# Kernel optimization log

Measured on AMD Instinct MI355X. Metric: run time of the kernel, lower is better.

The kernel has to match this reference:

```python
import jax, jax.numpy as jnp
import numpy as np

B, NN, HIS, MSG = 16, 1000, 12, 64
NODE_DIM, EDGE_DIM, META_DIM = 32, 16, 128
GAT_DIM = HIS * MSG            # 768
META_IN = NODE_DIM + GAT_DIM   # 800
N = B * NN                     # 16000 total nodes
E = 128000
NEG_SLOPE = 0.2


def setup_inputs() -> dict:
    key = jax.random.key(0)
    ks = jax.random.split(key, 16)
    def glorot(k, shape):
        fan_in = shape[0]
        lim = 1.0 / np.sqrt(fan_in)
        return jax.random.uniform(k, shape, jnp.float32, -lim, lim)
    return {
        "node_feature": jax.random.normal(ks[0], (B, NN, NODE_DIM), jnp.float32),
        "edge_attr": jax.random.normal(ks[1], (E, EDGE_DIM), jnp.float32),
        "message_feature": jax.random.normal(ks[2], (B, NN, HIS, MSG), jnp.float32),
        "edge_index": jax.random.randint(ks[3], (2, E), 0, N, jnp.int64) if jax.config.jax_enable_x64 else jax.random.randint(ks[3], (2, E), 0, N, jnp.int32),
        # node_learner / edge_learner
        "W_node": glorot(ks[4], (NODE_DIM, NODE_DIM)),
        "b_node": jnp.zeros((NODE_DIM,), jnp.float32),
        "W_edge": glorot(ks[5], (EDGE_DIM, EDGE_DIM)),
        "b_edge": jnp.zeros((EDGE_DIM,), jnp.float32),
        # GATConv(768, 768, heads=1, concat=False)
        "W_gat": glorot(ks[6], (GAT_DIM, GAT_DIM)),
        "att_src": glorot(ks[7], (GAT_DIM,)) * 0.1,
        "att_dst": glorot(ks[8], (GAT_DIM,)) * 0.1,
        "b_gat": jnp.zeros((GAT_DIM,), jnp.float32),
        # GNNConv([meta_in, meta_dim], dim=edge_dim)
        "W_nbr": glorot(ks[9], (2 * META_IN + EDGE_DIM, META_DIM)),
        "b_nbr": jnp.zeros((META_DIM,), jnp.float32),
        "W_self": glorot(ks[10], (META_IN, META_DIM)),
        "b_self": jnp.zeros((META_DIM,), jnp.float32),
    }


def reference(node_feature, edge_attr, message_feature, edge_index,
              W_node, b_node, W_edge, b_edge,
              W_gat, att_src, att_dst, b_gat,
              W_nbr, b_nbr, W_self, b_self):
    src, dst = edge_index[0], edge_index[1]  # j -> i

    # node / edge learners
    nf = (node_feature @ W_node + b_node).reshape(-1, NODE_DIM)        # [N, 32]
    ea = edge_attr @ W_edge + b_edge                                   # [E, 16]
    mf = message_feature.reshape(-1, GAT_DIM)                          # [N, 768]

    # --- GATConv (1 head, concat=False, add_self_loops=True, eval: no dropout) ---
    loops = jnp.arange(N, dtype=src.dtype)
    src_sl = jnp.concatenate([src, loops])
    dst_sl = jnp.concatenate([dst, loops])
    h = mf @ W_gat                                                     # [N, 768]
    a_src = h @ att_src                                                # [N]
    a_dst = h @ att_dst                                                # [N]
    alpha = jax.nn.leaky_relu(a_src[src_sl] + a_dst[dst_sl], NEG_SLOPE)  # [E+N]
    amax = jax.ops.segment_max(alpha, dst_sl, num_segments=N)
    ex = jnp.exp(alpha - amax[dst_sl])
    denom = jax.ops.segment_sum(ex, dst_sl, num_segments=N)
    coef = ex / denom[dst_sl]
    gat_out = jax.ops.segment_sum(h[src_sl] * coef[:, None], dst_sl, num_segments=N) + b_gat

    # --- meta input + GNNConv (aggr='add', batch_norm=False) ---
    x = jnp.concatenate([gat_out, nf], axis=-1)                        # [N, 800]
    z = jnp.concatenate([x[dst], x[src], ea], axis=-1)                 # [E, 1616]
    msg = z @ W_nbr + b_nbr                                            # [E, 128]
    agg = jax.ops.segment_sum(msg, dst, num_segments=N)                # [N, 128]
    out = agg + x @ W_self + b_self                                    # [N, 128]
    return out.reshape(-1, NN, META_DIM)                               # [B, 1000, 128]
```

## Files before the change

kernel.cpp:

```cpp
#include <hip/hip_runtime.h>

#define N_NODES 16000
#define N_EDGES 128000
#define GATD 768
#define NODED 32
#define EDGED 16
#define METAIN 800
#define METAD 128
#define YCOLS 384

typedef short s16x8 __attribute__((ext_vector_type(8)));
typedef float f32x4v __attribute__((ext_vector_type(4)));

__device__ __forceinline__ unsigned short f2bf(float f){
    unsigned u = __float_as_uint(f);
    return (unsigned short)((u + 0x7fffu + ((u >> 16) & 1u)) >> 16);
}

__device__ __forceinline__ void gload16(const void* g, void* l){
    __builtin_amdgcn_global_load_lds((const __attribute__((address_space(1))) void*)g,
                                     (__attribute__((address_space(3))) void*)l, 16, 0, 0);
}


__global__ __launch_bounds__(256) void conv_bf16_kernel(const float* __restrict__ in,
                                                        unsigned short* __restrict__ out, int n8){
    int i = blockIdx.x*256 + threadIdx.x;
    if (i >= n8) return;
    const float4* p = reinterpret_cast<const float4*>(in) + (size_t)i*2;
    float4 a = p[0], b = p[1];
    union { unsigned short u[8]; s16x8 v; } o;
    o.u[0]=f2bf(a.x); o.u[1]=f2bf(a.y); o.u[2]=f2bf(a.z); o.u[3]=f2bf(a.w);
    o.u[4]=f2bf(b.x); o.u[5]=f2bf(b.y); o.u[6]=f2bf(b.z); o.u[7]=f2bf(b.w);
    reinterpret_cast<s16x8*>(out)[i] = o.v;
}

__global__ __launch_bounds__(256) void wgat_t_kernel(const float* __restrict__ W_gat,
                                                     unsigned short* __restrict__ WgT){
    int idx = blockIdx.x*256 + threadIdx.x;
    int c = idx / GATD, k = idx % GATD;
    WgT[idx] = f2bf(W_gat[(size_t)k*GATD + c]);
}

__global__ __launch_bounds__(256) void wcat_t_kernel(const float* __restrict__ W_nbr,
                                                     const float* __restrict__ W_self,
                                                     unsigned short* __restrict__ WcatT){
    int idx = blockIdx.x*256 + threadIdx.x;
    int c = idx / METAIN, k = idx % METAIN;
    float v;
    if (c < 128)      v = W_nbr[(size_t)k*METAD + c];
    else if (c < 256) v = W_nbr[(size_t)(800+k)*METAD + (c-128)];
    else              v = W_self[(size_t)k*METAD + (c-256)];
    WcatT[idx] = f2bf(v);
}


__global__ __launch_bounds__(256) void ea_kernel(const float* __restrict__ edge_attr,
                                                 const float* __restrict__ W_edge,
                                                 const float* __restrict__ b_edge,
                                                 float* __restrict__ ea_lin){
    __shared__ float We[256];
    __shared__ float be[16];
    int tid = threadIdx.x;
    We[tid] = W_edge[tid];
    if (tid < 16) be[tid] = b_edge[tid];
    __syncthreads();
    int idx = blockIdx.x*256 + tid;
    int e = idx >> 4, j = idx & 15;
    const float* row = edge_attr + (size_t)e*EDGED;
    float s = be[j];
    #pragma unroll
    for (int k = 0; k < 16; ++k) s += row[k] * We[k*16 + j];
    ea_lin[idx] = s;
}

__global__ __launch_bounds__(256) void nf_kernel(const float* __restrict__ node_feature,
                                                 const float* __restrict__ W_node,
                                                 const float* __restrict__ b_node,
                                                 unsigned short* __restrict__ x_bf){
    __shared__ float Wn[1024];
    __shared__ float bn[32];
    int tid = threadIdx.x;
    for (int i = tid; i < 1024; i += 256) Wn[i] = node_feature ? W_node[i] : 0.f;
    if (tid < 32) bn[tid] = b_node[tid];
    __syncthreads();
    int idx = blockIdx.x*256 + tid;
    int n = idx >> 5, j = idx & 31;
    const float* row = node_feature + (size_t)n*NODED;
    float s = bn[j];
    #pragma unroll
    for (int k = 0; k < 32; ++k) s += row[k] * Wn[k*32 + j];
    x_bf[(size_t)n*METAIN + GATD + j] = f2bf(s);
}


__global__ __launch_bounds__(256) void deg_kernel(const int* __restrict__ dst, int* __restrict__ deg){
    int e = blockIdx.x*256 + threadIdx.x;
    atomicAdd(&deg[dst[e]], 1);
}

__global__ __launch_bounds__(1024) void scan_kernel(const int* __restrict__ deg,
                                                    int* __restrict__ rowstart,
                                                    int* __restrict__ cursor){
    __shared__ int part[1024];
    int t = threadIdx.x;
    int base = t * 16;
    int local[16];
    int s = 0;
    #pragma unroll
    for (int k = 0; k < 16; ++k){
        int idx = base + k;
        int v = (idx < N_NODES) ? deg[idx] : 0;
        local[k] = s; s += v;
    }
    part[t] = s;
    __syncthreads();
    for (int off = 1; off < 1024; off <<= 1){
        int v = 0;
        if (t >= off) v = part[t-off];
        __syncthreads();
        if (t >= off) part[t] += v;
        __syncthreads();
    }
    int excl = (t == 0) ? 0 : part[t-1];
    #pragma unroll
    for (int k = 0; k < 16; ++k){
        int idx = base + k;
        if (idx < N_NODES){ int rs = excl + local[k]; rowstart[idx] = rs; cursor[idx] = rs; }
    }
    if (t == 1023) rowstart[N_NODES] = part[1023];
}

__global__ __launch_bounds__(256) void csr_kernel(const int* __restrict__ dst,
                                                  int* __restrict__ cursor,
                                                  int* __restrict__ csr){
    int e = blockIdx.x*256 + threadIdx.x;
    int p = atomicAdd(&cursor[dst[e]], 1);
    csr[p] = e;
}


__global__ __launch_bounds__(256) void mfma_gemm_kernel(const unsigned short* __restrict__ A,
                                                        const unsigned short* __restrict__ Bt,
                                                        float* __restrict__ C,
                                                        int Ncols, int K){
    __shared__ __align__(16) unsigned short As[128*32];
    __shared__ __align__(16) unsigned short Bs[128*32];
    int tid = threadIdx.x;
    int wave = tid >> 6, lane = tid & 63;
    int rowBase = blockIdx.y * 128, colBase = blockIdx.x * 128;
    const unsigned short* gA = A + (size_t)(rowBase + (tid>>2))*K + (tid&3)*8;
    const unsigned short* gB = Bt + (size_t)(colBase + (tid>>2))*K + (tid&3)*8;
    char* lA = (char*)As + tid*16;
    char* lB = (char*)Bs + tid*16;
    int r0 = (wave>>1)*64, c0 = (wave&1)*64;
    int rl = lane & 15, koff = (lane>>4)*8;
    f32x4v acc[4][4] = {};
    for (int k0 = 0; k0 < K; k0 += 32){
        __syncthreads();
        gload16(gA + k0,                     lA);
        gload16(gA + (size_t)64*K + k0,      lA + 4096);
        gload16(gB + k0,                     lB);
        gload16(gB + (size_t)64*K + k0,      lB + 4096);
        __syncthreads();
        s16x8 af[4], bfr[4];
        #pragma unroll
        for (int mi = 0; mi < 4; ++mi)
            af[mi] = *reinterpret_cast<const s16x8*>(&As[(r0 + mi*16 + rl)*32 + koff]);
        #pragma unroll
        for (int ni = 0; ni < 4; ++ni)
            bfr[ni] = *reinterpret_cast<const s16x8*>(&Bs[(c0 + ni*16 + rl)*32 + koff]);
        #pragma unroll
        for (int mi = 0; mi < 4; ++mi)
            #pragma unroll
            for (int ni = 0; ni < 4; ++ni)
                acc[mi][ni] = __builtin_amdgcn_mfma_f32_16x16x32_bf16(af[mi], bfr[ni], acc[mi][ni], 0, 0, 0);
    }
    int orow = rowBase + r0 + (lane>>4)*4;
    int ocol = colBase + c0 + rl;
    #pragma unroll
    for (int mi = 0; mi < 4; ++mi)
        #pragma unroll
        for (int ni = 0; ni < 4; ++ni){
            float* cp = C + (size_t)(orow + mi*16)*Ncols + ocol + ni*16;
            #pragma unroll
            for (int j = 0; j < 4; ++j) cp[(size_t)j*Ncols] = acc[mi][ni][j];
        }
}


__global__ __launch_bounds__(256) void attn_dots_kernel(const float* __restrict__ h,
                                                        const float* __restrict__ att_src,
                                                        const float* __restrict__ att_dst,
                                                        float* __restrict__ a_src,
                                                        float* __restrict__ a_dst){
    int w = threadIdx.x >> 6, lane = threadIdx.x & 63;
    int n = blockIdx.x*4 + w;
    const float* hr = h + (size_t)n*GATD;
    float s = 0.f, d = 0.f;
    #pragma unroll
    for (int j = lane; j < GATD; j += 64){
        float hv = hr[j];
        s += hv * att_src[j];
        d += hv * att_dst[j];
    }
    #pragma unroll
    for (int off = 32; off; off >>= 1){ s += __shfl_xor(s, off); d += __shfl_xor(d, off); }
    if (lane == 0){ a_src[n] = s; a_dst[n] = d; }
}

__global__ __launch_bounds__(256) void edge_ex_kernel(const int* __restrict__ src,
                                                      const int* __restrict__ dst,
                                                      const float* __restrict__ a_src,
                                                      const float* __restrict__ a_dst,
                                                      float* __restrict__ ex,
                                                      float* __restrict__ denom){
    int e = blockIdx.x*256 + threadIdx.x;
    int s = src[e], d = dst[e];
    float al = a_src[s] + a_dst[d];
    al = al > 0.f ? al : 0.2f*al;
    float ee = expf(al);
    ex[e] = ee;
    atomicAdd(&denom[d], ee);
}

__global__ __launch_bounds__(256) void gat_gather_kernel(const float* __restrict__ h,
                                                         const float* __restrict__ ex,
                                                         const float* __restrict__ a_src,
                                                         const float* __restrict__ a_dst,
                                                         const float* __restrict__ denom,
                                                         const float* __restrict__ b_gat,
                                                         const int* __restrict__ src,
                                                         const int* __restrict__ rowstart,
                                                         const int* __restrict__ csr,
                                                         unsigned short* __restrict__ x_bf){
    __shared__ int   s_src[64];
    __shared__ float s_ex[64];
    int i = blockIdx.x, t = threadIdx.x;
    float asd = a_src[i] + a_dst[i];
    asd = asd > 0.f ? asd : 0.2f*asd;
    float ex_self = expf(asd);
    const float* hi = h + (size_t)i*GATD;
    float acc0 = ex_self*hi[t], acc1 = ex_self*hi[t+256], acc2 = ex_self*hi[t+512];
    int rs = rowstart[i], re = rowstart[i+1];
    for (int p = rs; p < re; p += 64){
        int cnt = min(64, re - p);
        __syncthreads();
        if (t < cnt){ int e = csr[p+t]; s_src[t] = src[e]; s_ex[t] = ex[e]; }
        __syncthreads();
        for (int j = 0; j < cnt; ++j){
            float w = s_ex[j];
            const float* hs = h + (size_t)s_src[j]*GATD;
            acc0 += w*hs[t]; acc1 += w*hs[t+256]; acc2 += w*hs[t+512];
        }
    }
    float inv = 1.f / (denom[i] + ex_self);
    unsigned short* xr = x_bf + (size_t)i*METAIN;
    xr[t]     = f2bf(acc0*inv + b_gat[t]);
    xr[t+256] = f2bf(acc1*inv + b_gat[t+256]);
    xr[t+512] = f2bf(acc2*inv + b_gat[t+512]);
}


__global__ __launch_bounds__(128) void out_gather_kernel(const float* __restrict__ y,
                                                         const float* __restrict__ ea_lin,
                                                         const float* __restrict__ W_nbr,
                                                         const float* __restrict__ b_nbr,
                                                         const float* __restrict__ b_self,
                                                         const int* __restrict__ src,
                                                         const int* __restrict__ rowstart,
                                                         const int* __restrict__ csr,
                                                         float* __restrict__ out){
    __shared__ float W3[16*128];
    __shared__ int   s_src[32];
    __shared__ int   s_eid[32];
    __shared__ float s_ea[32*16];
    int i = blockIdx.x, c = threadIdx.x;
    #pragma unroll
    for (int k = 0; k < 16; ++k) W3[k*128 + c] = W_nbr[(size_t)(1600+k)*METAD + c];
    int rs = rowstart[i], re = rowstart[i+1];
    int deg = re - rs;
    float acc = 0.f;
    for (int p = rs; p < re; p += 32){
        int cnt = min(32, re - p);
        __syncthreads();
        if (c < cnt){ int e = csr[p+c]; s_eid[c] = e; s_src[c] = src[e]; }
        __syncthreads();
        for (int idx = c; idx < cnt*16; idx += 128){
            int j = idx >> 4, k = idx & 15;
            s_ea[idx] = ea_lin[(size_t)s_eid[j]*EDGED + k];
        }
        __syncthreads();
        for (int j = 0; j < cnt; ++j){
            acc += y[(size_t)s_src[j]*YCOLS + 128 + c];
            float ez = 0.f;
            #pragma unroll
            for (int k = 0; k < 16; ++k) ez += s_ea[j*16 + k] * W3[k*128 + c];
            acc += ez;
        }
    }
    float y1 = y[(size_t)i*YCOLS + c];
    float ys = y[(size_t)i*YCOLS + 256 + c];
    float outv = (float)deg * (y1 + b_nbr[c]) + acc + ys + b_self[c];
    out[(size_t)i*METAD + c] = outv;
}


extern "C" void kernel_launch(void* const* d_in, const int* in_sizes, int n_in,
                              void* d_out, int out_size, void* d_ws, size_t ws_size,
                              hipStream_t stream){
    const float* node_feature    = (const float*)d_in[0];
    const float* edge_attr       = (const float*)d_in[1];
    const float* message_feature = (const float*)d_in[2];
    const int*   edge_index      = (const int*)d_in[3];
    const float* W_node = (const float*)d_in[4];
    const float* b_node = (const float*)d_in[5];
    const float* W_edge = (const float*)d_in[6];
    const float* b_edge = (const float*)d_in[7];
    const float* W_gat  = (const float*)d_in[8];
    const float* att_src= (const float*)d_in[9];
    const float* att_dst= (const float*)d_in[10];
    const float* b_gat  = (const float*)d_in[11];
    const float* W_nbr  = (const float*)d_in[12];
    const float* b_nbr  = (const float*)d_in[13];
    const float* W_self = (const float*)d_in[14];
    const float* b_self = (const float*)d_in[15];
    float* out = (float*)d_out;

    char* wsb = (char*)d_ws;
    size_t off = 0;
    auto walloc = [&](size_t bytes)->void*{
        void* p = wsb + off;
        off = (off + bytes + 511) & ~(size_t)511;
        return p;
    };
    float* h            = (float*)walloc((size_t)N_NODES*GATD*4);
    float* y            = (float*)walloc((size_t)N_NODES*YCOLS*4);
    float* ea_lin       = (float*)walloc((size_t)N_EDGES*EDGED*4);
    unsigned short* A_bf  = (unsigned short*)walloc((size_t)N_NODES*GATD*2);
    unsigned short* x_bf  = (unsigned short*)walloc((size_t)N_NODES*METAIN*2);
    unsigned short* WgT   = (unsigned short*)walloc((size_t)GATD*GATD*2);
    unsigned short* WcatT = (unsigned short*)walloc((size_t)YCOLS*METAIN*2);
    float* ex     = (float*)walloc((size_t)N_EDGES*4);
    float* a_src  = (float*)walloc((size_t)N_NODES*4);
    float* a_dst  = (float*)walloc((size_t)N_NODES*4);
    float* denom  = (float*)walloc((size_t)N_NODES*4);
    int* deg      = (int*)walloc((size_t)N_NODES*4);
    int* rowstart = (int*)walloc((size_t)(N_NODES+1)*4);
    int* cursor   = (int*)walloc((size_t)N_NODES*4);
    int* csr      = (int*)walloc((size_t)N_EDGES*4);

    const int* src = edge_index;
    const int* dst = edge_index + N_EDGES;

    hipMemsetAsync(deg,   0, (size_t)N_NODES*4, stream);
    hipMemsetAsync(denom, 0, (size_t)N_NODES*4, stream);

    conv_bf16_kernel<<<(N_NODES*GATD/8 + 255)/256, 256, 0, stream>>>(message_feature, A_bf, N_NODES*GATD/8);
    wgat_t_kernel<<<(GATD*GATD)/256, 256, 0, stream>>>(W_gat, WgT);
    wcat_t_kernel<<<(YCOLS*METAIN)/256, 256, 0, stream>>>(W_nbr, W_self, WcatT);

    ea_kernel<<<(N_EDGES*EDGED)/256, 256, 0, stream>>>(edge_attr, W_edge, b_edge, ea_lin);
    nf_kernel<<<(N_NODES*NODED)/256, 256, 0, stream>>>(node_feature, W_node, b_node, x_bf);
    deg_kernel<<<N_EDGES/256, 256, 0, stream>>>(dst, deg);
    scan_kernel<<<1, 1024, 0, stream>>>(deg, rowstart, cursor);
    csr_kernel<<<N_EDGES/256, 256, 0, stream>>>(dst, cursor, csr);

    mfma_gemm_kernel<<<dim3(GATD/128, N_NODES/128), 256, 0, stream>>>(A_bf, WgT, h, GATD, GATD);
    attn_dots_kernel<<<N_NODES/4, 256, 0, stream>>>(h, att_src, att_dst, a_src, a_dst);
    edge_ex_kernel<<<N_EDGES/256, 256, 0, stream>>>(src, dst, a_src, a_dst, ex, denom);
    gat_gather_kernel<<<N_NODES, 256, 0, stream>>>(h, ex, a_src, a_dst, denom, b_gat, src, rowstart, csr, x_bf);

    mfma_gemm_kernel<<<dim3(YCOLS/128, N_NODES/128), 256, 0, stream>>>(x_bf, WcatT, y, YCOLS, METAIN);
    out_gather_kernel<<<N_NODES, 128, 0, stream>>>(y, ea_lin, W_nbr, b_nbr, b_self, src, rowstart, csr, out);
}
```

Before: 368.0 us.

## Store GAT projection in bf16 and fuse edge softmax into wave-per-node gather

The first GEMM now writes h in bf16 rather than fp32, which halves the traffic for the attention dot products and the random-row gather. The separate edge_ex kernel, with its atomic denominator accumulation and its ex/denom buffers, is removed. Edge exponentials and the softmax denominator are instead computed inside the gather, which now uses one wavefront per destination node and broadcasts neighbour data through shuffles instead of shared memory and block syncs. The cost is bf16 rounding of h before the attention logits and aggregation, and fewer threads per node in the gather.

```diff
diff --git a/kernel.cpp b/kernel.cpp
--- a/kernel.cpp
+++ b/kernel.cpp
@@ -16,6 +16,7 @@
     unsigned u = __float_as_uint(f);
     return (unsigned short)((u + 0x7fffu + ((u >> 16) & 1u)) >> 16);
 }
+__device__ __forceinline__ float us2f(unsigned short u){ return __uint_as_float(((unsigned)u)<<16); }
 
 __device__ __forceinline__ void gload16(const void* g, void* l){
     __builtin_amdgcn_global_load_lds((const __attribute__((address_space(1))) void*)g,
@@ -81,7 +82,7 @@
     __shared__ float Wn[1024];
     __shared__ float bn[32];
     int tid = threadIdx.x;
-    for (int i = tid; i < 1024; i += 256) Wn[i] = node_feature ? W_node[i] : 0.f;
+    for (int i = tid; i < 1024; i += 256) Wn[i] = W_node[i];
     if (tid < 32) bn[tid] = b_node[tid];
     __syncthreads();
     int idx = blockIdx.x*256 + tid;
@@ -140,9 +141,11 @@
 }
 
 
+template<bool BFOUT>
 __global__ __launch_bounds__(256) void mfma_gemm_kernel(const unsigned short* __restrict__ A,
                                                         const unsigned short* __restrict__ Bt,
-                                                        float* __restrict__ C,
+                                                        float* __restrict__ Cf,
+                                                        unsigned short* __restrict__ Cb,
                                                         int Ncols, int K){
     __shared__ __align__(16) unsigned short As[128*32];
     __shared__ __align__(16) unsigned short Bs[128*32];
@@ -182,83 +185,98 @@
     for (int mi = 0; mi < 4; ++mi)
         #pragma unroll
         for (int ni = 0; ni < 4; ++ni){
-            float* cp = C + (size_t)(orow + mi*16)*Ncols + ocol + ni*16;
             #pragma unroll
-            for (int j = 0; j < 4; ++j) cp[(size_t)j*Ncols] = acc[mi][ni][j];
-        }
-}
-
-
-__global__ __launch_bounds__(256) void attn_dots_kernel(const float* __restrict__ h,
+            for (int j = 0; j < 4; ++j){
+                size_t idx = (size_t)(orow + mi*16 + j)*Ncols + ocol + ni*16;
+                if constexpr (BFOUT) Cb[idx] = f2bf(acc[mi][ni][j]);
+                else                 Cf[idx] = acc[mi][ni][j];
+            }
+        }
+}
+
+
+__global__ __launch_bounds__(256) void attn_dots_kernel(const unsigned short* __restrict__ h_bf,
                                                         const float* __restrict__ att_src,
                                                         const float* __restrict__ att_dst,
                                                         float* __restrict__ a_src,
                                                         float* __restrict__ a_dst){
     int w = threadIdx.x >> 6, lane = threadIdx.x & 63;
     int n = blockIdx.x*4 + w;
-    const float* hr = h + (size_t)n*GATD;
+    const unsigned short* hr = h_bf + (size_t)n*GATD;
     float s = 0.f, d = 0.f;
     #pragma unroll
-    for (int j = lane; j < GATD; j += 64){
-        float hv = hr[j];
-        s += hv * att_src[j];
-        d += hv * att_dst[j];
+    for (int c = 0; c < 3; ++c){
+        int o = c*256 + lane*4;
+        ushort4 v  = *reinterpret_cast<const ushort4*>(hr + o);
+        float4 as4 = *reinterpret_cast<const float4*>(att_src + o);
+        float4 ad4 = *reinterpret_cast<const float4*>(att_dst + o);
+        float f0 = us2f(v.x), f1 = us2f(v.y), f2 = us2f(v.z), f3 = us2f(v.w);
+        s += f0*as4.x + f1*as4.y + f2*as4.z + f3*as4.w;
+        d += f0*ad4.x + f1*ad4.y + f2*ad4.z + f3*ad4.w;
     }
     #pragma unroll
     for (int off = 32; off; off >>= 1){ s += __shfl_xor(s, off); d += __shfl_xor(d, off); }
     if (lane == 0){ a_src[n] = s; a_dst[n] = d; }
 }
 
-__global__ __launch_bounds__(256) void edge_ex_kernel(const int* __restrict__ src,
-                                                      const int* __restrict__ dst,
-                                                      const float* __restrict__ a_src,
-                                                      const float* __restrict__ a_dst,
-                                                      float* __restrict__ ex,
-                                                      float* __restrict__ denom){
-    int e = blockIdx.x*256 + threadIdx.x;
-    int s = src[e], d = dst[e];
-    float al = a_src[s] + a_dst[d];
-    al = al > 0.f ? al : 0.2f*al;
-    float ee = expf(al);
-    ex[e] = ee;
-    atomicAdd(&denom[d], ee);
-}
-
-__global__ __launch_bounds__(256) void gat_gather_kernel(const float* __restrict__ h,
-                                                         const float* __restrict__ ex,
+
+__global__ __launch_bounds__(256) void gat_gather_kernel(const unsigned short* __restrict__ h_bf,
                                                          const float* __restrict__ a_src,
                                                          const float* __restrict__ a_dst,
-                                                         const float* __restrict__ denom,
                                                          const float* __restrict__ b_gat,
                                                          const int* __restrict__ src,
                                                          const int* __restrict__ rowstart,
                                                          const int* __restrict__ csr,
                                                          unsigned short* __restrict__ x_bf){
-    __shared__ int   s_src[64];
-    __shared__ float s_ex[64];
-    int i = blockIdx.x, t = threadIdx.x;
-    float asd = a_src[i] + a_dst[i];
-    asd = asd > 0.f ? asd : 0.2f*asd;
-    float ex_self = expf(asd);
-    const float* hi = h + (size_t)i*GATD;
-    float acc0 = ex_self*hi[t], acc1 = ex_self*hi[t+256], acc2 = ex_self*hi[t+512];
+    int wv = threadIdx.x >> 6, lane = threadIdx.x & 63;
+    int i = blockIdx.x*4 + wv;
+    float adi = a_dst[i];
+    float al = a_src[i] + adi;
+    al = al > 0.f ? al : 0.2f*al;
+    float ex_self = expf(al);
+    const unsigned short* hi = h_bf + (size_t)i*GATD;
+    float acc[12];
+    #pragma unroll
+    for (int c = 0; c < 3; ++c){
+        ushort4 v = *reinterpret_cast<const ushort4*>(hi + c*256 + lane*4);
+        acc[c*4+0] = ex_self*us2f(v.x); acc[c*4+1] = ex_self*us2f(v.y);
+        acc[c*4+2] = ex_self*us2f(v.z); acc[c*4+3] = ex_self*us2f(v.w);
+    }
+    float dsum = ex_self;
     int rs = rowstart[i], re = rowstart[i+1];
     for (int p = rs; p < re; p += 64){
         int cnt = min(64, re - p);
-        __syncthreads();
-        if (t < cnt){ int e = csr[p+t]; s_src[t] = src[e]; s_ex[t] = ex[e]; }
-        __syncthreads();
+        int sv = 0; float ev = 0.f;
+        if (lane < cnt){
+            int e = csr[p+lane];
+            sv = src[e];
+            float a = a_src[sv] + adi;
+            a = a > 0.f ? a : 0.2f*a;
+            ev = expf(a);
+        }
         for (int j = 0; j < cnt; ++j){
-            float w = s_ex[j];
-            const float* hs = h + (size_t)s_src[j]*GATD;
-            acc0 += w*hs[t]; acc1 += w*hs[t+256]; acc2 += w*hs[t+512];
-        }
-    }
-    float inv = 1.f / (denom[i] + ex_self);
+            int   ss = __shfl(sv, j);
+            float ww = __shfl(ev, j);
+            dsum += ww;
+            const unsigned short* hs = h_bf + (size_t)ss*GATD;
+            #pragma unroll
+            for (int c = 0; c < 3; ++c){
+                ushort4 v = *reinterpret_cast<const ushort4*>(hs + c*256 + lane*4);
+                acc[c*4+0] += ww*us2f(v.x); acc[c*4+1] += ww*us2f(v.y);
+                acc[c*4+2] += ww*us2f(v.z); acc[c*4+3] += ww*us2f(v.w);
+            }
+        }
+    }
+    float inv = 1.f / dsum;
     unsigned short* xr = x_bf + (size_t)i*METAIN;
-    xr[t]     = f2bf(acc0*inv + b_gat[t]);
-    xr[t+256] = f2bf(acc1*inv + b_gat[t+256]);
-    xr[t+512] = f2bf(acc2*inv + b_gat[t+512]);
+    #pragma unroll
+    for (int c = 0; c < 3; ++c){
+        float4 bg = *reinterpret_cast<const float4*>(b_gat + c*256 + lane*4);
+        ushort4 o;
+        o.x = f2bf(acc[c*4+0]*inv + bg.x); o.y = f2bf(acc[c*4+1]*inv + bg.y);
+        o.z = f2bf(acc[c*4+2]*inv + bg.z); o.w = f2bf(acc[c*4+3]*inv + bg.w);
+        *reinterpret_cast<ushort4*>(xr + c*256 + lane*4) = o;
+    }
 }
 
 
@@ -334,17 +352,15 @@
         off = (off + bytes + 511) & ~(size_t)511;
         return p;
     };
-    float* h            = (float*)walloc((size_t)N_NODES*GATD*4);
-    float* y            = (float*)walloc((size_t)N_NODES*YCOLS*4);
-    float* ea_lin       = (float*)walloc((size_t)N_EDGES*EDGED*4);
+    unsigned short* h_bf  = (unsigned short*)walloc((size_t)N_NODES*GATD*2);
+    float* y              = (float*)walloc((size_t)N_NODES*YCOLS*4);
+    float* ea_lin         = (float*)walloc((size_t)N_EDGES*EDGED*4);
     unsigned short* A_bf  = (unsigned short*)walloc((size_t)N_NODES*GATD*2);
     unsigned short* x_bf  = (unsigned short*)walloc((size_t)N_NODES*METAIN*2);
     unsigned short* WgT   = (unsigned short*)walloc((size_t)GATD*GATD*2);
     unsigned short* WcatT = (unsigned short*)walloc((size_t)YCOLS*METAIN*2);
-    float* ex     = (float*)walloc((size_t)N_EDGES*4);
     float* a_src  = (float*)walloc((size_t)N_NODES*4);
     float* a_dst  = (float*)walloc((size_t)N_NODES*4);
-    float* denom  = (float*)walloc((size_t)N_NODES*4);
     int* deg      = (int*)walloc((size_t)N_NODES*4);
     int* rowstart = (int*)walloc((size_t)(N_NODES+1)*4);
     int* cursor   = (int*)walloc((size_t)N_NODES*4);
@@ -353,8 +369,7 @@
     const int* src = edge_index;
     const int* dst = edge_index + N_EDGES;
 
-    hipMemsetAsync(deg,   0, (size_t)N_NODES*4, stream);
-    hipMemsetAsync(denom, 0, (size_t)N_NODES*4, stream);
+    hipMemsetAsync(deg, 0, (size_t)N_NODES*4, stream);
 
     conv_bf16_kernel<<<(N_NODES*GATD/8 + 255)/256, 256, 0, stream>>>(message_feature, A_bf, N_NODES*GATD/8);
     wgat_t_kernel<<<(GATD*GATD)/256, 256, 0, stream>>>(W_gat, WgT);
@@ -366,11 +381,10 @@
     scan_kernel<<<1, 1024, 0, stream>>>(deg, rowstart, cursor);
     csr_kernel<<<N_EDGES/256, 256, 0, stream>>>(dst, cursor, csr);
 
-    mfma_gemm_kernel<<<dim3(GATD/128, N_NODES/128), 256, 0, stream>>>(A_bf, WgT, h, GATD, GATD);
-    attn_dots_kernel<<<N_NODES/4, 256, 0, stream>>>(h, att_src, att_dst, a_src, a_dst);
-    edge_ex_kernel<<<N_EDGES/256, 256, 0, stream>>>(src, dst, a_src, a_dst, ex, denom);
-    gat_gather_kernel<<<N_NODES, 256, 0, stream>>>(h, ex, a_src, a_dst, denom, b_gat, src, rowstart, csr, x_bf);
-
-    mfma_gemm_kernel<<<dim3(YCOLS/128, N_NODES/128), 256, 0, stream>>>(x_bf, WcatT, y, YCOLS, METAIN);
+    mfma_gemm_kernel<true><<<dim3(GATD/128, N_NODES/128), 256, 0, stream>>>(A_bf, WgT, nullptr, h_bf, GATD, GATD);
+    attn_dots_kernel<<<N_NODES/4, 256, 0, stream>>>(h_bf, att_src, att_dst, a_src, a_dst);
+    gat_gather_kernel<<<N_NODES/4, 256, 0, stream>>>(h_bf, a_src, a_dst, b_gat, src, rowstart, csr, x_bf);
+
+    mfma_gemm_kernel<false><<<dim3(YCOLS/128, N_NODES/128), 256, 0, stream>>>(x_bf, WcatT, y, nullptr, YCOLS, METAIN);
     out_gather_kernel<<<N_NODES, 128, 0, stream>>>(y, ea_lin, W_nbr, b_nbr, b_self, src, rowstart, csr, out);
 }
```

New measurement: 320.4 us. -12.9%, faster.
